# Optimization experiments

Hardware: AMD Instinct MI355X
Metric: run time of the kernel (lower is better)

## Reference

```python
import jax, jax.numpy as jnp
import numpy as np

THRESHOLD_PERCENTILE = 0.8  # init arg
B, H, W, C, N = 4, 256, 256, 128, 32


def _label_components(mask):
    """8-connected components via iterative min-label propagation.
    Background pixels get sentinel label BIG (== scipy label 0)."""
    h, w = mask.shape
    big = h * w
    init = jnp.where(mask, jnp.arange(big, dtype=jnp.int32).reshape(h, w), jnp.int32(big))

    def propagate(lbl):
        p = jnp.pad(lbl, 1, constant_values=big)
        # min over the 3x3 (8-connected incl. self) neighborhood
        nb = jnp.min(jnp.stack([p[di:di + h, dj:dj + w]
                                for di in range(3) for dj in range(3)]), axis=0)
        return jnp.where(mask, nb, jnp.int32(big))

    def cond(state):
        return ~state[1]

    def body(state):
        lbl, _ = state
        new = propagate(lbl)
        return new, jnp.all(new == lbl)

    lbl, _ = jax.lax.while_loop(cond, body, (init, jnp.array(False)))
    return lbl, jnp.int32(big)


def _merged_pairs_one(feat, centers):
    """feat: [H,W,C] float; centers: [N,2] int32. Returns merged-pair count."""
    h, w, c = feat.shape
    gt = feat[centers[:, 0], centers[:, 1]]                    # [N,C]
    flat = feat.reshape(-1, c)                                 # [HW,C]
    # euclidean cdist via norms (torch.cdist p=2)
    d2 = (jnp.sum(flat * flat, axis=1)[:, None]
          + jnp.sum(gt * gt, axis=1)[None, :]
          - 2.0 * flat @ gt.T)                                 # [HW,N]
    dists = jnp.sqrt(jnp.maximum(d2, 0.0))
    contrast = dists.min(axis=1).reshape(h, w)                 # [H,W]
    thr = jnp.percentile(contrast, THRESHOLD_PERCENTILE * 100.0)
    mask = contrast >= thr
    lbl, big = _label_components(mask)
    ids = lbl[centers[:, 0], centers[:, 1]]                    # [N]
    valid = ids != big                                         # scipy label > 0
    eq = (ids[:, None] == ids[None, :]) & valid[:, None]
    n = centers.shape[0]
    triu = jnp.triu(jnp.ones((n, n), dtype=bool), 1)           # i < j pairs
    return jnp.sum(eq & triu)


def setup_inputs() -> dict:
    key = jax.random.key(0)
    k1, k2 = jax.random.split(key)
    features = jax.random.normal(k1, (B, H, W, C), dtype=jnp.float32)
    gt_centers = jax.random.randint(k2, (B, N, 2), 0, H, dtype=jnp.int64)
    return {"features": features, "gt_centers": gt_centers}


def reference(features, gt_centers):
    centers = gt_centers.astype(jnp.int32)
    merged = jax.vmap(_merged_pairs_one)(features, centers)    # [B]
    n = centers.shape[1]
    total_pairs = features.shape[0] * (n * (n - 1) // 2)
    merge_rate = merged.sum().astype(jnp.float32) / jnp.float32(total_pairs)
    return merge_rate
```

## Files before the change

### kernel.cpp

```cpp
#include <hip/hip_runtime.h>
#include <stdint.h>

#define BB 4
#define HH 256
#define WW 256
#define CC 128
#define NN 32
#define NPIX (HH*WW)
#define RANK 52428u
#define TOTAL_PAIRS 1984.0f

#define OFF_SM      0
#define OFF_KEYS    4096
#define OFF_P       (OFF_KEYS + BB*NPIX*4)

typedef __attribute__((ext_vector_type(8))) short short8;
typedef __attribute__((ext_vector_type(4))) float f32x4;

__device__ __forceinline__ void split3(float f, short &hi, short &mid, short &lo) {
    uint32_t u  = __float_as_uint(f);
    uint32_t hb = u & 0xffff0000u;
    hi = (short)(hb >> 16);
    float r1 = f - __uint_as_float(hb);
    uint32_t mb = __float_as_uint(r1) & 0xffff0000u;
    mid = (short)(mb >> 16);
    float r2 = r1 - __uint_as_float(mb);
    lo = (short)(__float_as_uint(r2) >> 16);
}

__device__ __forceinline__ uint32_t qbin_of(uint32_t keybits) {
    float f = __uint_as_float(keybits);
    return (uint32_t)fminf(f * 128.0f, 65535.0f);
}

__global__ __launch_bounds__(256) void k_d2mfma(const float* __restrict__ feat,
        const int* __restrict__ centers, uint32_t* __restrict__ keys) {
    __shared__ short gB[12288];
    __shared__ float gpart[32][8];
    __shared__ float gnormL[32];
    int b = blockIdx.y;
    int tid = threadIdx.x;

    {
        int n = tid & 31, j0 = tid >> 5;
        int cy = centers[(b*NN + n)*2 + 0];
        int cx = centers[(b*NN + n)*2 + 1];
        const float* gp = feat + ((size_t)(b << 16) + cy*WW + cx)*CC + j0*16;
        int tt = n >> 4, lane16 = n & 15, kk = j0 >> 1, qbase = (j0 & 1)*2;
        float ss = 0.f;
        #pragma unroll
        for (int hh = 0; hh < 2; hh++) {
            short8 vhi, vmid, vlo;
            #pragma unroll
            for (int u = 0; u < 8; u++) {
                float f = gp[hh*8 + u];
                ss = fmaf(f, f, ss);
                short a, bm, c; split3(f, a, bm, c);
                vhi[u] = a; vmid[u] = bm; vlo[u] = c;
            }
            int lane = (qbase + hh)*16 + lane16;
            int off = (tt*4 + kk)*512 + lane*8;
            *(short8*)&gB[off]        = vhi;
            *(short8*)&gB[off + 4096] = vmid;
            *(short8*)&gB[off + 8192] = vlo;
        }
        gpart[n][j0] = ss;
    }
    __syncthreads();
    if (tid < 32) {
        float s = 0.f;
        #pragma unroll
        for (int j = 0; j < 8; j++) s += gpart[tid][j];
        gnormL[tid] = s;
    }
    __syncthreads();

    int wv = tid >> 6, L = tid & 63;
    int m = L & 15, q = L >> 4;
    float gn0 = gnormL[m];
    float gn1 = gnormL[16 + m];

    for (int it = 0; it < 4; it++) {
        int p0 = blockIdx.x*256 + (wv*4 + it)*16;
        const float* fp = feat + ((size_t)(b << 16) + p0 + m)*CC + q*8;

        f32x4 acc[2] = {{0.f,0.f,0.f,0.f},{0.f,0.f,0.f,0.f}};
        float fn = 0.f;

        #pragma unroll
        for (int kk = 0; kk < 4; kk++) {
            float4 fa = *(const float4*)(fp + kk*32);
            float4 fb = *(const float4*)(fp + kk*32 + 4);
            float fs[8] = {fa.x,fa.y,fa.z,fa.w,fb.x,fb.y,fb.z,fb.w};
            short8 ahi, amid, alo;
            #pragma unroll
            for (int j = 0; j < 8; j++) {
                float f = fs[j];
                fn = fmaf(f, f, fn);
                short hh, md, lw; split3(f, hh, md, lw);
                ahi[j] = hh; amid[j] = md; alo[j] = lw;
            }
            #pragma unroll
            for (int t = 0; t < 2; t++) {
                int off = (t*4 + kk)*512 + L*8;
                short8 bhi = *(const short8*)&gB[off];
                short8 bmd = *(const short8*)&gB[off + 4096];
                short8 blo = *(const short8*)&gB[off + 8192];
                acc[t] = __builtin_amdgcn_mfma_f32_16x16x32_bf16(ahi,  bhi, acc[t], 0,0,0);
                acc[t] = __builtin_amdgcn_mfma_f32_16x16x32_bf16(ahi,  bmd, acc[t], 0,0,0);
                acc[t] = __builtin_amdgcn_mfma_f32_16x16x32_bf16(amid, bhi, acc[t], 0,0,0);
                acc[t] = __builtin_amdgcn_mfma_f32_16x16x32_bf16(ahi,  blo, acc[t], 0,0,0);
                acc[t] = __builtin_amdgcn_mfma_f32_16x16x32_bf16(amid, bmd, acc[t], 0,0,0);
                acc[t] = __builtin_amdgcn_mfma_f32_16x16x32_bf16(alo,  bhi, acc[t], 0,0,0);
            }
        }

        fn += __shfl_xor(fn, 16);
        fn += __shfl_xor(fn, 32);

        float vmin[4];
        #pragma unroll
        for (int r = 0; r < 4; r++) {
            float fnr = __shfl(fn, q*4 + r);
            float d0 = fnr + gn0 - 2.f*acc[0][r];
            float d1 = fnr + gn1 - 2.f*acc[1][r];
            float v = fminf(d0, d1);
            v = fminf(v, __shfl_xor(v, 1));
            v = fminf(v, __shfl_xor(v, 2));
            v = fminf(v, __shfl_xor(v, 4));
            v = fminf(v, __shfl_xor(v, 8));
            vmin[r] = v;
        }
        if (m < 4) {
            float v = (m==0) ? vmin[0] : (m==1) ? vmin[1] : (m==2) ? vmin[2] : vmin[3];
            if (!(v > 0.f)) v = 0.f;
            keys[(size_t)(b << 16) + p0 + q*4 + m] = __float_as_uint(v);
        }
    }
}

__global__ __launch_bounds__(1024) void k_selthr(const uint32_t* __restrict__ keys,
                                                 uint32_t* __restrict__ sm) {
    int b = blockIdx.x, t = threadIdx.x;
    __shared__ uint32_t h1[1024];
    __shared__ uint32_t h2[64];
    __shared__ uint32_t wsum[16];
    __shared__ uint32_t sT1, sR1, sT, sR2, scnt;
    __shared__ uint32_t cand[8192];
    const uint4* kb = (const uint4*)(keys + (b << 16));

    h1[t] = 0;
    if (t < 64) h2[t] = 0;
    if (t == 0) scnt = 0;
    __syncthreads();

    for (int i = t; i < NPIX/4; i += 1024) {
        uint4 k = kb[i];
        atomicAdd(&h1[qbin_of(k.x) >> 6], 1u);
        atomicAdd(&h1[qbin_of(k.y) >> 6], 1u);
        atomicAdd(&h1[qbin_of(k.z) >> 6], 1u);
        atomicAdd(&h1[qbin_of(k.w) >> 6], 1u);
    }
    __syncthreads();

    int lane = t & 63, w = t >> 6;
    uint32_t s = h1[t];
    uint32_t inc = s;
    #pragma unroll
    for (int off = 1; off < 64; off <<= 1) {
        uint32_t nb = __shfl_up((int)inc, off);
        if (lane >= off) inc += nb;
    }
    if (lane == 63) wsum[w] = inc;
    __syncthreads();
    if (t < 16) {
        uint32_t v = wsum[t];
        #pragma unroll
        for (int off = 1; off < 16; off <<= 1) {
            uint32_t nb = __shfl_up((int)v, off);
            if (t >= off) v += nb;
        }
        wsum[t] = v;
    }
    __syncthreads();
    uint32_t pre = ((w == 0) ? 0u : wsum[w-1]) + inc - s;
    if (pre <= RANK && RANK < pre + s) { sT1 = (uint32_t)t; sR1 = RANK - pre; }
    __syncthreads();
    uint32_t T1 = sT1, r1 = sR1;

    for (int i = t; i < NPIX/4; i += 1024) {
        uint4 k = kb[i];
        uint32_t q0 = qbin_of(k.x); if ((q0 >> 6) == T1) atomicAdd(&h2[q0 & 63u], 1u);
        uint32_t q1 = qbin_of(k.y); if ((q1 >> 6) == T1) atomicAdd(&h2[q1 & 63u], 1u);
        uint32_t q2 = qbin_of(k.z); if ((q2 >> 6) == T1) atomicAdd(&h2[q2 & 63u], 1u);
        uint32_t q3 = qbin_of(k.w); if ((q3 >> 6) == T1) atomicAdd(&h2[q3 & 63u], 1u);
    }
    __syncthreads();
    if (t < 64) {
        uint32_t s2 = h2[t];
        uint32_t inc2 = s2;
        #pragma unroll
        for (int off = 1; off < 64; off <<= 1) {
            uint32_t nb = __shfl_up((int)inc2, off);
            if (t >= off) inc2 += nb;
        }
        uint32_t pre2 = inc2 - s2;
        if (pre2 <= r1 && r1 < pre2 + s2) { sT = (T1 << 6) | (uint32_t)t; sR2 = r1 - pre2; }
    }
    __syncthreads();
    uint32_t T = sT, r2 = sR2;

    for (int i = t; i < NPIX/4; i += 1024) {
        uint4 k = kb[i];
        if (qbin_of(k.x) == T) { uint32_t p = atomicAdd(&scnt, 1u); if (p < 8192u) cand[p] = k.x; }
        if (qbin_of(k.y) == T) { uint32_t p = atomicAdd(&scnt, 1u); if (p < 8192u) cand[p] = k.y; }
        if (qbin_of(k.z) == T) { uint32_t p = atomicAdd(&scnt, 1u); if (p < 8192u) cand[p] = k.z; }
        if (qbin_of(k.w) == T) { uint32_t p = atomicAdd(&scnt, 1u); if (p < 8192u) cand[p] = k.w; }
    }
    __syncthreads();
    uint32_t K = scnt; if (K > 8192u) K = 8192u;

    for (uint32_t i = t; i < K; i += 1024) {
        uint32_t v = cand[i];
        uint32_t less = 0, eq = 0;
        for (uint32_t j = 0; j < K; j++) { uint32_t x = cand[j]; less += (x < v); eq += (x == v); }
        if (less <= r2 && r2 < less + eq) sm[12 + b] = v;
    }
}

__global__ __launch_bounds__(256) void k_initrun(const uint32_t* __restrict__ keys,
        const uint32_t* __restrict__ sm, int* __restrict__ P) {
    int b = blockIdx.y;
    int row = blockIdx.x, x = threadIdx.x;
    int p = row*256 + x;
    uint32_t thr = sm[12 + b];
    bool msk = keys[(b << 16) + p] >= thr;

    __shared__ int wmax[4];
    int lane = x & 63, w = x >> 6;
    int v = msk ? -1 : x;
    #pragma unroll
    for (int off = 1; off < 64; off <<= 1) {
        int nb = __shfl_up(v, off);
        if (lane >= off) v = max(v, nb);
    }
    if (lane == 63) wmax[w] = v;
    __syncthreads();
    int acc = v;
    for (int i = 0; i < w; i++) acc = max(acc, wmax[i]);
    P[(b << 16) + p] = msk ? (row*256 + acc + 1) : -1;
}

__device__ __forceinline__ int uf_find(int* P, int x) {
    while (true) {
        int p = P[x];
        if (p == x) return x;
        int gp = P[p];
        if (gp != p) P[x] = gp;
        x = gp;
    }
}
__device__ __forceinline__ void uf_unite(int* P, int a, int b) {
    while (true) {
        a = uf_find(P, a);
        b = uf_find(P, b);
        if (a == b) return;
        if (a > b) { int t = a; a = b; b = t; }
        int old = atomicCAS(&P[b], b, a);
        if (old == b) return;
        b = old;
    }
}
__global__ __launch_bounds__(256) void k_union(int* __restrict__ Pg) {
    int b = blockIdx.y;
    int p = blockIdx.x*256 + threadIdx.x;
    int* P = Pg + (b << 16);
    if (P[p] == -1) return;
    int y = p >> 8, x = p & 255;
    if (y == 0) return;
    bool ul = (x > 0)   && P[p-WW-1] != -1;
    bool uu =              P[p-WW]   != -1;
    bool ur = (x < 255) && P[p-WW+1] != -1;
    if (ul)        uf_unite(P, p, p-WW-1);
    if (uu && !ul) uf_unite(P, p, p-WW);
    if (ur && !uu) uf_unite(P, p, p-WW+1);
}

__global__ void k_pairs_fin(const int* __restrict__ centers, int* __restrict__ Pg,
                            float* __restrict__ out) {
    __shared__ int ids[BB*NN];
    __shared__ int total;
    int t = threadIdx.x;
    if (t == 0) total = 0;
    __syncthreads();
    if (t < BB*NN) {
        int b = t >> 5;
        int cy = centers[t*2 + 0];
        int cx = centers[t*2 + 1];
        int p = cy*WW + cx;
        const int* P = Pg + (b << 16);
        int id = P[p];
        if (id != -1) {
            int x = p;
            while (true) { int q = P[x]; if (q == x) break; x = q; }
            id = x;
        }
        ids[t] = id;
    }
    __syncthreads();
    int cnt = 0;
    if (t < BB*NN) {
        int b = t >> 5, n = t & 31;
        int id = ids[t];
        if (id != -1) for (int j = n+1; j < NN; j++) cnt += (ids[b*NN + j] == id);
    }
    if (cnt) atomicAdd(&total, cnt);
    __syncthreads();
    if (t == 0) out[0] = (float)total / TOTAL_PAIRS;
}

extern "C" void kernel_launch(void* const* d_in, const int* in_sizes, int n_in,
                              void* d_out, int out_size, void* d_ws, size_t ws_size,
                              hipStream_t stream) {
    const float* feat  = (const float*)d_in[0];
    const int* centers = (const int*)d_in[1];
    float* out         = (float*)d_out;
    char* ws           = (char*)d_ws;

    uint32_t* sm   = (uint32_t*)(ws + OFF_SM);
    uint32_t* keys = (uint32_t*)(ws + OFF_KEYS);
    int*      Pg   = (int*)(ws + OFF_P);

    dim3 gridPix(NPIX/256, BB);

    k_d2mfma    <<<gridPix, 256, 0, stream>>>(feat, centers, keys);
    k_selthr    <<<BB, 1024, 0, stream>>>(keys, sm);
    k_initrun   <<<gridPix, 256, 0, stream>>>(keys, sm, Pg);
    k_union     <<<gridPix, 256, 0, stream>>>(Pg);
    k_pairs_fin <<<1, 256, 0, stream>>>(centers, Pg, out);
}
```

Measured before the change: 232.4 us.

## Fuse histogram into distance kernel and merge tail stages into cooperative kernel

The coarse threshold histogram is now built inside the distance kernel using shared-memory bins flushed to global, so the key array no longer needs a separate pass. The single-block-per-batch threshold selection, mask/run init, union and pair counting are merged into one cooperative kernel of 1024 blocks with grid syncs between phases. The fine histogram and candidate gathering are spread across many blocks, and the exact rank search is restricted to candidates in the final bin. This cuts launch overhead and removes the serialized 4-block selection kernel. In exchange it adds a memset, global atomics and grid-wide barriers, and it requires all 1024 blocks to be co-resident.

```diff
diff --git a/kernel.cpp b/kernel.cpp
--- a/kernel.cpp
+++ b/kernel.cpp
@@ -1,5 +1,8 @@
 #include <hip/hip_runtime.h>
+#include <hip/hip_cooperative_groups.h>
 #include <stdint.h>
+
+namespace cg = cooperative_groups;
 
 #define BB 4
 #define HH 256
@@ -9,10 +12,16 @@
 #define NPIX (HH*WW)
 #define RANK 52428u
 #define TOTAL_PAIRS 1984.0f
-
-#define OFF_SM      0
-#define OFF_KEYS    4096
-#define OFF_P       (OFF_KEYS + BB*NPIX*4)
+#define CAND_MAX 8192u
+
+#define OFF_KEYS 0
+#define OFF_P    (BB*NPIX*4)
+#define OFF_HIST (OFF_P + BB*NPIX*4)
+#define OFF_FINE (OFF_HIST + BB*1024*4)
+#define OFF_CNT  (OFF_FINE + BB*64*4)
+#define OFF_THR  (OFF_CNT + 64)
+#define OFF_CAND (OFF_THR + 64)
+#define ZERO_BYTES (BB*1024*4 + BB*64*4 + 64)
 
 typedef __attribute__((ext_vector_type(8))) short short8;
 typedef __attribute__((ext_vector_type(4))) float f32x4;
@@ -34,12 +43,17 @@
 }
 
 __global__ __launch_bounds__(256) void k_d2mfma(const float* __restrict__ feat,
-        const int* __restrict__ centers, uint32_t* __restrict__ keys) {
+        const int* __restrict__ centers, uint32_t* __restrict__ keys,
+        uint32_t* __restrict__ hist) {
     __shared__ short gB[12288];
     __shared__ float gpart[32][8];
     __shared__ float gnormL[32];
+    __shared__ uint32_t lhist[1024];
     int b = blockIdx.y;
     int tid = threadIdx.x;
+
+    #pragma unroll
+    for (int j = 0; j < 4; j++) lhist[tid + j*256] = 0u;
 
     {
         int n = tid & 31, j0 = tid >> 5;
@@ -134,121 +148,19 @@
         if (m < 4) {
             float v = (m==0) ? vmin[0] : (m==1) ? vmin[1] : (m==2) ? vmin[2] : vmin[3];
             if (!(v > 0.f)) v = 0.f;
-            keys[(size_t)(b << 16) + p0 + q*4 + m] = __float_as_uint(v);
-        }
-    }
-}
-
-__global__ __launch_bounds__(1024) void k_selthr(const uint32_t* __restrict__ keys,
-                                                 uint32_t* __restrict__ sm) {
-    int b = blockIdx.x, t = threadIdx.x;
-    __shared__ uint32_t h1[1024];
-    __shared__ uint32_t h2[64];
-    __shared__ uint32_t wsum[16];
-    __shared__ uint32_t sT1, sR1, sT, sR2, scnt;
-    __shared__ uint32_t cand[8192];
-    const uint4* kb = (const uint4*)(keys + (b << 16));
-
-    h1[t] = 0;
-    if (t < 64) h2[t] = 0;
-    if (t == 0) scnt = 0;
+            uint32_t kb = __float_as_uint(v);
+            keys[(size_t)(b << 16) + p0 + q*4 + m] = kb;
+            atomicAdd(&lhist[qbin_of(kb) >> 6], 1u);
+        }
+    }
+
     __syncthreads();
-
-    for (int i = t; i < NPIX/4; i += 1024) {
-        uint4 k = kb[i];
-        atomicAdd(&h1[qbin_of(k.x) >> 6], 1u);
-        atomicAdd(&h1[qbin_of(k.y) >> 6], 1u);
-        atomicAdd(&h1[qbin_of(k.z) >> 6], 1u);
-        atomicAdd(&h1[qbin_of(k.w) >> 6], 1u);
-    }
-    __syncthreads();
-
-    int lane = t & 63, w = t >> 6;
-    uint32_t s = h1[t];
-    uint32_t inc = s;
     #pragma unroll
-    for (int off = 1; off < 64; off <<= 1) {
-        uint32_t nb = __shfl_up((int)inc, off);
-        if (lane >= off) inc += nb;
-    }
-    if (lane == 63) wsum[w] = inc;
-    __syncthreads();
-    if (t < 16) {
-        uint32_t v = wsum[t];
-        #pragma unroll
-        for (int off = 1; off < 16; off <<= 1) {
-            uint32_t nb = __shfl_up((int)v, off);
-            if (t >= off) v += nb;
-        }
-        wsum[t] = v;
-    }
-    __syncthreads();
-    uint32_t pre = ((w == 0) ? 0u : wsum[w-1]) + inc - s;
-    if (pre <= RANK && RANK < pre + s) { sT1 = (uint32_t)t; sR1 = RANK - pre; }
-    __syncthreads();
-    uint32_t T1 = sT1, r1 = sR1;
-
-    for (int i = t; i < NPIX/4; i += 1024) {
-        uint4 k = kb[i];
-        uint32_t q0 = qbin_of(k.x); if ((q0 >> 6) == T1) atomicAdd(&h2[q0 & 63u], 1u);
-        uint32_t q1 = qbin_of(k.y); if ((q1 >> 6) == T1) atomicAdd(&h2[q1 & 63u], 1u);
-        uint32_t q2 = qbin_of(k.z); if ((q2 >> 6) == T1) atomicAdd(&h2[q2 & 63u], 1u);
-        uint32_t q3 = qbin_of(k.w); if ((q3 >> 6) == T1) atomicAdd(&h2[q3 & 63u], 1u);
-    }
-    __syncthreads();
-    if (t < 64) {
-        uint32_t s2 = h2[t];
-        uint32_t inc2 = s2;
-        #pragma unroll
-        for (int off = 1; off < 64; off <<= 1) {
-            uint32_t nb = __shfl_up((int)inc2, off);
-            if (t >= off) inc2 += nb;
-        }
-        uint32_t pre2 = inc2 - s2;
-        if (pre2 <= r1 && r1 < pre2 + s2) { sT = (T1 << 6) | (uint32_t)t; sR2 = r1 - pre2; }
-    }
-    __syncthreads();
-    uint32_t T = sT, r2 = sR2;
-
-    for (int i = t; i < NPIX/4; i += 1024) {
-        uint4 k = kb[i];
-        if (qbin_of(k.x) == T) { uint32_t p = atomicAdd(&scnt, 1u); if (p < 8192u) cand[p] = k.x; }
-        if (qbin_of(k.y) == T) { uint32_t p = atomicAdd(&scnt, 1u); if (p < 8192u) cand[p] = k.y; }
-        if (qbin_of(k.z) == T) { uint32_t p = atomicAdd(&scnt, 1u); if (p < 8192u) cand[p] = k.z; }
-        if (qbin_of(k.w) == T) { uint32_t p = atomicAdd(&scnt, 1u); if (p < 8192u) cand[p] = k.w; }
-    }
-    __syncthreads();
-    uint32_t K = scnt; if (K > 8192u) K = 8192u;
-
-    for (uint32_t i = t; i < K; i += 1024) {
-        uint32_t v = cand[i];
-        uint32_t less = 0, eq = 0;
-        for (uint32_t j = 0; j < K; j++) { uint32_t x = cand[j]; less += (x < v); eq += (x == v); }
-        if (less <= r2 && r2 < less + eq) sm[12 + b] = v;
-    }
-}
-
-__global__ __launch_bounds__(256) void k_initrun(const uint32_t* __restrict__ keys,
-        const uint32_t* __restrict__ sm, int* __restrict__ P) {
-    int b = blockIdx.y;
-    int row = blockIdx.x, x = threadIdx.x;
-    int p = row*256 + x;
-    uint32_t thr = sm[12 + b];
-    bool msk = keys[(b << 16) + p] >= thr;
-
-    __shared__ int wmax[4];
-    int lane = x & 63, w = x >> 6;
-    int v = msk ? -1 : x;
-    #pragma unroll
-    for (int off = 1; off < 64; off <<= 1) {
-        int nb = __shfl_up(v, off);
-        if (lane >= off) v = max(v, nb);
-    }
-    if (lane == 63) wmax[w] = v;
-    __syncthreads();
-    int acc = v;
-    for (int i = 0; i < w; i++) acc = max(acc, wmax[i]);
-    P[(b << 16) + p] = msk ? (row*256 + acc + 1) : -1;
+    for (int j = 0; j < 4; j++) {
+        int bin = tid + j*256;
+        uint32_t hv = lhist[bin];
+        if (hv) atomicAdd(&hist[(b << 10) + bin], hv);
+    }
 }
 
 __device__ __forceinline__ int uf_find(int* P, int x) {
@@ -271,52 +183,154 @@
         b = old;
     }
 }
-__global__ __launch_bounds__(256) void k_union(int* __restrict__ Pg) {
-    int b = blockIdx.y;
-    int p = blockIdx.x*256 + threadIdx.x;
-    int* P = Pg + (b << 16);
-    if (P[p] == -1) return;
-    int y = p >> 8, x = p & 255;
-    if (y == 0) return;
-    bool ul = (x > 0)   && P[p-WW-1] != -1;
-    bool uu =              P[p-WW]   != -1;
-    bool ur = (x < 255) && P[p-WW+1] != -1;
-    if (ul)        uf_unite(P, p, p-WW-1);
-    if (uu && !ul) uf_unite(P, p, p-WW);
-    if (ur && !uu) uf_unite(P, p, p-WW+1);
-}
-
-__global__ void k_pairs_fin(const int* __restrict__ centers, int* __restrict__ Pg,
-                            float* __restrict__ out) {
+
+__global__ __launch_bounds__(256, 4) void k_tail(const int* __restrict__ centers,
+        const uint32_t* __restrict__ keys, const uint32_t* __restrict__ hist,
+        uint32_t* __restrict__ fineh, uint32_t* __restrict__ cnt,
+        uint32_t* __restrict__ cand, uint32_t* __restrict__ thr_sm,
+        int* __restrict__ Pg, float* __restrict__ out) {
+    cg::grid_group grid = cg::this_grid();
+    int bid = blockIdx.x;
+    int b = bid >> 8, rr = bid & 255;
+    int tid = threadIdx.x;
+
+    __shared__ uint32_t swsum[4];
+    __shared__ uint32_t sT1, sR1, sT, sR2;
+    __shared__ int swmax[4];
     __shared__ int ids[BB*NN];
-    __shared__ int total;
-    int t = threadIdx.x;
-    if (t == 0) total = 0;
-    __syncthreads();
-    if (t < BB*NN) {
-        int b = t >> 5;
-        int cy = centers[t*2 + 0];
-        int cx = centers[t*2 + 1];
-        int p = cy*WW + cx;
-        const int* P = Pg + (b << 16);
-        int id = P[p];
-        if (id != -1) {
-            int x = p;
-            while (true) { int q = P[x]; if (q == x) break; x = q; }
-            id = x;
-        }
-        ids[t] = id;
-    }
-    __syncthreads();
-    int cnt = 0;
-    if (t < BB*NN) {
-        int b = t >> 5, n = t & 31;
-        int id = ids[t];
-        if (id != -1) for (int j = n+1; j < NN; j++) cnt += (ids[b*NN + j] == id);
-    }
-    if (cnt) atomicAdd(&total, cnt);
-    __syncthreads();
-    if (t == 0) out[0] = (float)total / TOTAL_PAIRS;
+    __shared__ int stotal;
+
+    if (rr < 32) {
+        const uint4* hb = (const uint4*)(hist + (b << 10));
+        uint4 h = hb[tid];
+        uint32_t s = h.x + h.y + h.z + h.w;
+        int lane = tid & 63, w = tid >> 6;
+        uint32_t inc = s;
+        #pragma unroll
+        for (int off = 1; off < 64; off <<= 1) {
+            uint32_t nb = __shfl_up((int)inc, off);
+            if (lane >= off) inc += nb;
+        }
+        if (lane == 63) swsum[w] = inc;
+        __syncthreads();
+        uint32_t prew = 0;
+        for (int i = 0; i < w; i++) prew += swsum[i];
+        uint32_t pre = prew + inc - s;
+        uint32_t cs[4] = {h.x, h.y, h.z, h.w};
+        #pragma unroll
+        for (int j = 0; j < 4; j++) {
+            if (pre <= RANK && RANK < pre + cs[j]) { sT1 = 4u*(uint32_t)tid + (uint32_t)j; sR1 = RANK - pre; }
+            pre += cs[j];
+        }
+        __syncthreads();
+        uint32_t T1 = sT1;
+
+        const uint4* kb = (const uint4*)(keys + ((size_t)b << 16)) + (rr << 9);
+        #pragma unroll
+        for (int i = 0; i < 2; i++) {
+            uint4 k = kb[tid + i*256];
+            uint32_t q;
+            #define PROC_KEY(X) { q = qbin_of(X); if ((q >> 6) == T1) { \
+                atomicAdd(&fineh[(b << 6) + (q & 63u)], 1u); \
+                uint32_t pp = atomicAdd(&cnt[b], 1u); \
+                if (pp < CAND_MAX) cand[b*CAND_MAX + pp] = (X); } }
+            PROC_KEY(k.x) PROC_KEY(k.y) PROC_KEY(k.z) PROC_KEY(k.w)
+            #undef PROC_KEY
+        }
+    }
+    grid.sync();
+
+    if (rr == 0) {
+        uint32_t T1 = sT1, r1 = sR1;
+        if (tid < 64) {
+            uint32_t s2 = fineh[(b << 6) + tid];
+            uint32_t inc2 = s2;
+            #pragma unroll
+            for (int off = 1; off < 64; off <<= 1) {
+                uint32_t nb = __shfl_up((int)inc2, off);
+                if (tid >= off) inc2 += nb;
+            }
+            uint32_t pre2 = inc2 - s2;
+            if (pre2 <= r1 && r1 < pre2 + s2) { sT = (T1 << 6) | (uint32_t)tid; sR2 = r1 - pre2; }
+        }
+        __syncthreads();
+        uint32_t T = sT, r2 = sR2;
+        uint32_t K = cnt[b]; if (K > CAND_MAX) K = CAND_MAX;
+        const uint32_t* cd = cand + b*CAND_MAX;
+        for (uint32_t i = tid; i < K; i += 256) {
+            uint32_t v = cd[i];
+            if (qbin_of(v) != T) continue;
+            uint32_t less = 0, eq = 0;
+            for (uint32_t j = 0; j < K; j++) {
+                uint32_t x = cd[j];
+                if (qbin_of(x) == T) { less += (x < v); eq += (x == v); }
+            }
+            if (less <= r2 && r2 < less + eq) thr_sm[b] = v;
+        }
+    }
+    grid.sync();
+
+    {
+        uint32_t thrv = thr_sm[b];
+        int p = (rr << 8) + tid;
+        bool msk = keys[((size_t)b << 16) + p] >= thrv;
+        int lane = tid & 63, w = tid >> 6;
+        int v = msk ? -1 : tid;
+        #pragma unroll
+        for (int off = 1; off < 64; off <<= 1) {
+            int nb = __shfl_up(v, off);
+            if (lane >= off) v = max(v, nb);
+        }
+        if (lane == 63) swmax[w] = v;
+        __syncthreads();
+        int acc = v;
+        for (int i = 0; i < w; i++) acc = max(acc, swmax[i]);
+        Pg[((size_t)b << 16) + p] = msk ? ((rr << 8) + acc + 1) : -1;
+    }
+    grid.sync();
+
+    if (rr > 0) {
+        int* P = Pg + ((size_t)b << 16);
+        int p = (rr << 8) + tid;
+        if (P[p] != -1) {
+            bool ul = (tid > 0)   && P[p-WW-1] != -1;
+            bool uu =                P[p-WW]   != -1;
+            bool ur = (tid < 255) && P[p-WW+1] != -1;
+            if (ul)        uf_unite(P, p, p-WW-1);
+            if (uu && !ul) uf_unite(P, p, p-WW);
+            if (ur && !uu) uf_unite(P, p, p-WW+1);
+        }
+    }
+    grid.sync();
+
+    if (bid == 0) {
+        if (tid == 0) stotal = 0;
+        __syncthreads();
+        if (tid < BB*NN) {
+            int bb = tid >> 5;
+            int cy = centers[tid*2 + 0];
+            int cx = centers[tid*2 + 1];
+            int p = cy*WW + cx;
+            const int* P = Pg + ((size_t)bb << 16);
+            int id = P[p];
+            if (id != -1) {
+                int x = p;
+                while (true) { int q2 = P[x]; if (q2 == x) break; x = q2; }
+                id = x;
+            }
+            ids[tid] = id;
+        }
+        __syncthreads();
+        int c2 = 0;
+        if (tid < BB*NN) {
+            int bb = tid >> 5, n = tid & 31;
+            int id = ids[tid];
+            if (id != -1) for (int j = n+1; j < NN; j++) c2 += (ids[bb*NN + j] == id);
+        }
+        if (c2) atomicAdd(&stotal, c2);
+        __syncthreads();
+        if (tid == 0) out[0] = (float)stotal / TOTAL_PAIRS;
+    }
 }
 
 extern "C" void kernel_launch(void* const* d_in, const int* in_sizes, int n_in,
@@ -327,15 +341,20 @@
     float* out         = (float*)d_out;
     char* ws           = (char*)d_ws;
 
-    uint32_t* sm   = (uint32_t*)(ws + OFF_SM);
-    uint32_t* keys = (uint32_t*)(ws + OFF_KEYS);
-    int*      Pg   = (int*)(ws + OFF_P);
+    uint32_t* keys  = (uint32_t*)(ws + OFF_KEYS);
+    int*      Pg    = (int*)(ws + OFF_P);
+    uint32_t* hist  = (uint32_t*)(ws + OFF_HIST);
+    uint32_t* fineh = (uint32_t*)(ws + OFF_FINE);
+    uint32_t* cnt   = (uint32_t*)(ws + OFF_CNT);
+    uint32_t* thr   = (uint32_t*)(ws + OFF_THR);
+    uint32_t* cand  = (uint32_t*)(ws + OFF_CAND);
+
+    hipMemsetAsync(ws + OFF_HIST, 0, ZERO_BYTES, stream);
 
     dim3 gridPix(NPIX/256, BB);
-
-    k_d2mfma    <<<gridPix, 256, 0, stream>>>(feat, centers, keys);
-    k_selthr    <<<BB, 1024, 0, stream>>>(keys, sm);
-    k_initrun   <<<gridPix, 256, 0, stream>>>(keys, sm, Pg);
-    k_union     <<<gridPix, 256, 0, stream>>>(Pg);
-    k_pairs_fin <<<1, 256, 0, stream>>>(centers, Pg, out);
-}
+    k_d2mfma<<<gridPix, 256, 0, stream>>>(feat, centers, keys, hist);
+
+    void* args[] = { (void*)&centers, (void*)&keys, (void*)&hist, (void*)&fineh,
+                     (void*)&cnt, (void*)&cand, (void*)&thr, (void*)&Pg, (void*)&out };
+    hipLaunchCooperativeKernel((const void*)k_tail, dim3(HH*BB), dim3(256), args, 0u, stream);
+}
```

After: 747.9 us. 3.22x slower.

## Fuse coarse histogram into distance kernel and cut selection passes over keys

Applied to the files above, without the earlier changes.

The coarse 1024-bin histogram of contrast keys is now built in the distance kernel, using a shared-memory histogram per block that is flushed to global memory with atomics, so the selection kernel no longer makes its first full pass over the keys. The selection kernel merges the fine-histogram pass with candidate collection for the whole coarse bin, then filters those candidates down to the exact fine bin before the quadratic rank search. This removes two of the three full key scans done by only four blocks, at the cost of an extra memset, per-pixel LDS atomics in the distance kernel, and a larger candidate buffer that could overflow if a coarse bin holds more than 8192 keys.

```diff
diff --git a/kernel.cpp b/kernel.cpp
--- a/kernel.cpp
+++ b/kernel.cpp
@@ -9,10 +9,13 @@
 #define NPIX (HH*WW)
 #define RANK 52428u
 #define TOTAL_PAIRS 1984.0f
-
-#define OFF_SM      0
-#define OFF_KEYS    4096
-#define OFF_P       (OFF_KEYS + BB*NPIX*4)
+#define CAND_MAX 8192u
+
+#define OFF_KEYS 0
+#define OFF_P    (BB*NPIX*4)
+#define OFF_HIST (OFF_P + BB*NPIX*4)
+#define OFF_THR  (OFF_HIST + BB*1024*4)
+#define ZERO_BYTES (BB*1024*4)
 
 typedef __attribute__((ext_vector_type(8))) short short8;
 typedef __attribute__((ext_vector_type(4))) float f32x4;
@@ -34,12 +37,17 @@
 }
 
 __global__ __launch_bounds__(256) void k_d2mfma(const float* __restrict__ feat,
-        const int* __restrict__ centers, uint32_t* __restrict__ keys) {
+        const int* __restrict__ centers, uint32_t* __restrict__ keys,
+        uint32_t* __restrict__ hist) {
     __shared__ short gB[12288];
     __shared__ float gpart[32][8];
     __shared__ float gnormL[32];
+    __shared__ uint32_t lhist[1024];
     int b = blockIdx.y;
     int tid = threadIdx.x;
+
+    #pragma unroll
+    for (int j = 0; j < 4; j++) lhist[tid + j*256] = 0u;
 
     {
         int n = tid & 31, j0 = tid >> 5;
@@ -134,37 +142,35 @@
         if (m < 4) {
             float v = (m==0) ? vmin[0] : (m==1) ? vmin[1] : (m==2) ? vmin[2] : vmin[3];
             if (!(v > 0.f)) v = 0.f;
-            keys[(size_t)(b << 16) + p0 + q*4 + m] = __float_as_uint(v);
-        }
+            uint32_t kb = __float_as_uint(v);
+            keys[(size_t)(b << 16) + p0 + q*4 + m] = kb;
+            atomicAdd(&lhist[qbin_of(kb) >> 6], 1u);
+        }
+    }
+
+    __syncthreads();
+    #pragma unroll
+    for (int j = 0; j < 4; j++) {
+        int bin = tid + j*256;
+        uint32_t hv = lhist[bin];
+        if (hv) atomicAdd(&hist[(b << 10) + bin], hv);
     }
 }
 
 __global__ __launch_bounds__(1024) void k_selthr(const uint32_t* __restrict__ keys,
-                                                 uint32_t* __restrict__ sm) {
+        const uint32_t* __restrict__ hist, uint32_t* __restrict__ thr_sm) {
     int b = blockIdx.x, t = threadIdx.x;
-    __shared__ uint32_t h1[1024];
-    __shared__ uint32_t h2[64];
     __shared__ uint32_t wsum[16];
-    __shared__ uint32_t sT1, sR1, sT, sR2, scnt;
-    __shared__ uint32_t cand[8192];
-    const uint4* kb = (const uint4*)(keys + (b << 16));
-
-    h1[t] = 0;
-    if (t < 64) h2[t] = 0;
-    if (t == 0) scnt = 0;
-    __syncthreads();
-
-    for (int i = t; i < NPIX/4; i += 1024) {
-        uint4 k = kb[i];
-        atomicAdd(&h1[qbin_of(k.x) >> 6], 1u);
-        atomicAdd(&h1[qbin_of(k.y) >> 6], 1u);
-        atomicAdd(&h1[qbin_of(k.z) >> 6], 1u);
-        atomicAdd(&h1[qbin_of(k.w) >> 6], 1u);
-    }
-    __syncthreads();
+    __shared__ uint32_t sT1, sR1, sT, sR2, scnt, scnt2;
+    __shared__ uint32_t fh[64];
+    __shared__ uint32_t cand[CAND_MAX];
+    __shared__ uint32_t cand2[2048];
+
+    if (t < 64) fh[t] = 0;
+    if (t == 0) { scnt = 0; scnt2 = 0; }
 
     int lane = t & 63, w = t >> 6;
-    uint32_t s = h1[t];
+    uint32_t s = hist[(b << 10) + t];
     uint32_t inc = s;
     #pragma unroll
     for (int off = 1; off < 64; off <<= 1) {
@@ -188,16 +194,21 @@
     __syncthreads();
     uint32_t T1 = sT1, r1 = sR1;
 
+    const uint4* kb = (const uint4*)(keys + ((size_t)b << 16));
     for (int i = t; i < NPIX/4; i += 1024) {
         uint4 k = kb[i];
-        uint32_t q0 = qbin_of(k.x); if ((q0 >> 6) == T1) atomicAdd(&h2[q0 & 63u], 1u);
-        uint32_t q1 = qbin_of(k.y); if ((q1 >> 6) == T1) atomicAdd(&h2[q1 & 63u], 1u);
-        uint32_t q2 = qbin_of(k.z); if ((q2 >> 6) == T1) atomicAdd(&h2[q2 & 63u], 1u);
-        uint32_t q3 = qbin_of(k.w); if ((q3 >> 6) == T1) atomicAdd(&h2[q3 & 63u], 1u);
-    }
-    __syncthreads();
+        uint32_t q;
+        #define PROC_KEY(X) { q = qbin_of(X); if ((q >> 6) == T1) { \
+            atomicAdd(&fh[q & 63u], 1u); \
+            uint32_t p = atomicAdd(&scnt, 1u); \
+            if (p < CAND_MAX) cand[p] = (X); } }
+        PROC_KEY(k.x) PROC_KEY(k.y) PROC_KEY(k.z) PROC_KEY(k.w)
+        #undef PROC_KEY
+    }
+    __syncthreads();
+
     if (t < 64) {
-        uint32_t s2 = h2[t];
+        uint32_t s2 = fh[t];
         uint32_t inc2 = s2;
         #pragma unroll
         for (int off = 1; off < 64; off <<= 1) {
@@ -209,31 +220,29 @@
     }
     __syncthreads();
     uint32_t T = sT, r2 = sR2;
-
-    for (int i = t; i < NPIX/4; i += 1024) {
-        uint4 k = kb[i];
-        if (qbin_of(k.x) == T) { uint32_t p = atomicAdd(&scnt, 1u); if (p < 8192u) cand[p] = k.x; }
-        if (qbin_of(k.y) == T) { uint32_t p = atomicAdd(&scnt, 1u); if (p < 8192u) cand[p] = k.y; }
-        if (qbin_of(k.z) == T) { uint32_t p = atomicAdd(&scnt, 1u); if (p < 8192u) cand[p] = k.z; }
-        if (qbin_of(k.w) == T) { uint32_t p = atomicAdd(&scnt, 1u); if (p < 8192u) cand[p] = k.w; }
-    }
-    __syncthreads();
-    uint32_t K = scnt; if (K > 8192u) K = 8192u;
+    uint32_t K = scnt; if (K > CAND_MAX) K = CAND_MAX;
 
     for (uint32_t i = t; i < K; i += 1024) {
         uint32_t v = cand[i];
+        if (qbin_of(v) == T) { uint32_t p = atomicAdd(&scnt2, 1u); if (p < 2048u) cand2[p] = v; }
+    }
+    __syncthreads();
+    uint32_t K2 = scnt2; if (K2 > 2048u) K2 = 2048u;
+
+    for (uint32_t i = t; i < K2; i += 1024) {
+        uint32_t v = cand2[i];
         uint32_t less = 0, eq = 0;
-        for (uint32_t j = 0; j < K; j++) { uint32_t x = cand[j]; less += (x < v); eq += (x == v); }
-        if (less <= r2 && r2 < less + eq) sm[12 + b] = v;
+        for (uint32_t j = 0; j < K2; j++) { uint32_t x = cand2[j]; less += (x < v); eq += (x == v); }
+        if (less <= r2 && r2 < less + eq) thr_sm[b] = v;
     }
 }
 
 __global__ __launch_bounds__(256) void k_initrun(const uint32_t* __restrict__ keys,
-        const uint32_t* __restrict__ sm, int* __restrict__ P) {
+        const uint32_t* __restrict__ thr_sm, int* __restrict__ P) {
     int b = blockIdx.y;
     int row = blockIdx.x, x = threadIdx.x;
     int p = row*256 + x;
-    uint32_t thr = sm[12 + b];
+    uint32_t thr = thr_sm[b];
     bool msk = keys[(b << 16) + p] >= thr;
 
     __shared__ int wmax[4];
@@ -327,15 +336,17 @@
     float* out         = (float*)d_out;
     char* ws           = (char*)d_ws;
 
-    uint32_t* sm   = (uint32_t*)(ws + OFF_SM);
     uint32_t* keys = (uint32_t*)(ws + OFF_KEYS);
     int*      Pg   = (int*)(ws + OFF_P);
+    uint32_t* hist = (uint32_t*)(ws + OFF_HIST);
+    uint32_t* thr  = (uint32_t*)(ws + OFF_THR);
+
+    hipMemsetAsync(ws + OFF_HIST, 0, ZERO_BYTES, stream);
 
     dim3 gridPix(NPIX/256, BB);
-
-    k_d2mfma    <<<gridPix, 256, 0, stream>>>(feat, centers, keys);
-    k_selthr    <<<BB, 1024, 0, stream>>>(keys, sm);
-    k_initrun   <<<gridPix, 256, 0, stream>>>(keys, sm, Pg);
+    k_d2mfma    <<<gridPix, 256, 0, stream>>>(feat, centers, keys, hist);
+    k_selthr    <<<BB, 1024, 0, stream>>>(keys, hist, thr);
+    k_initrun   <<<gridPix, 256, 0, stream>>>(keys, thr, Pg);
     k_union     <<<gridPix, 256, 0, stream>>>(Pg);
     k_pairs_fin <<<1, 256, 0, stream>>>(centers, Pg, out);
 }
```

Result: no change. 232.8 us (+0.2%).
